# Optimization experiments

Measured on AMD Instinct MI355X. Metric: run time of the kernel, lower is better.

## Reference

```python
import jax, jax.numpy as jnp
import numpy as np

EMB_DIM = 2048
USER_DIM = 16 + 112  # 128
NUM_EXPERTS = 64
TOP_K = 8
N_TOKENS = 131072


def setup_inputs() -> dict:
    key = jax.random.key(0)
    k1, k2, k3, k4 = jax.random.split(key, 4)
    h = jax.random.normal(k1, (N_TOKENS, EMB_DIM), dtype=jnp.float32)
    u = jax.random.normal(k2, (N_TOKENS, USER_DIM), dtype=jnp.float32)
    fan_in = EMB_DIM + USER_DIM
    bound = 1.0 / np.sqrt(fan_in)
    # nn.Linear params: weight [E, emb+user], bias [E]
    W = jax.random.uniform(k3, (NUM_EXPERTS, fan_in), minval=-bound, maxval=bound, dtype=jnp.float32)
    b = jax.random.uniform(k4, (NUM_EXPERTS,), minval=-bound, maxval=bound, dtype=jnp.float32)
    return {"h": h, "u": u, "W": W, "b": b}


def reference(h, u, W, b):
    # router logits: concat along feature dim then linear -> [N, E]
    x = jnp.concatenate([h, u], axis=-1)
    g = jnp.einsum("nf,ef->ne", x, W) + b
    w = jax.nn.softmax(g, axis=-1)
    E = w.shape[-1]
    k = TOP_K
    if k is not None and k > 0 and k < E:
        _, idx = jax.lax.top_k(w, k)                      # [N, k] int32
        mask = jax.nn.one_hot(idx, E, dtype=w.dtype).sum(-2)  # [N, E] 0/1
        w = w * mask
        w = w / (w.sum(axis=-1, keepdims=True) + 1e-9)
    return w
```

## Files before the change

### kernel.cpp

```cpp
#include <hip/hip_runtime.h>
#include <math.h>

#define NTOK 131072
#define EMB  2048
#define UDIM 128
#define KDIM 2176
#define NE   64
#define TOPK 8

#define BM     128
#define BK     64
#define NCHUNK 34
#define NKSTEP 68
#define LSTR   65
#define MARGIN 1e-4f
#define WPLANE ((size_t)NKSTEP * 64 * 32)

typedef short bf16x8 __attribute__((ext_vector_type(8)));
typedef float f32x4  __attribute__((ext_vector_type(4)));

union FragU { uint4 u; bf16x8 v; };

__device__ __forceinline__ unsigned rnbf(unsigned u) {
    return u + 0x7FFFu + ((u >> 16) & 1u);
}

__device__ __forceinline__ void cvt8(const float4 a, const float4 b,
                                     uint4& hi, uint4& lo) {
    const float x[8] = {a.x, a.y, a.z, a.w, b.x, b.y, b.z, b.w};
    unsigned hh[4], ll[4];
    #pragma unroll
    for (int p = 0; p < 4; ++p) {
        const unsigned u0 = __float_as_uint(x[2*p]);
        const unsigned u1 = __float_as_uint(x[2*p+1]);
        const unsigned r0 = rnbf(u0), r1 = rnbf(u1);
        hh[p] = (r0 >> 16) | (r1 & 0xFFFF0000u);
        const float h0 = __uint_as_float(r0 & 0xFFFF0000u);
        const float h1 = __uint_as_float(r1 & 0xFFFF0000u);
        const unsigned s0 = rnbf(__float_as_uint(x[2*p]   - h0));
        const unsigned s1 = rnbf(__float_as_uint(x[2*p+1] - h1));
        ll[p] = (s0 >> 16) | (s1 & 0xFFFF0000u);
    }
    hi = make_uint4(hh[0], hh[1], hh[2], hh[3]);
    lo = make_uint4(ll[0], ll[1], ll[2], ll[3]);
}

__global__ __launch_bounds__(256)
void prep_w(const float* __restrict__ W,
            unsigned short* __restrict__ wh,
            unsigned short* __restrict__ wl)
{
    const int t = blockIdx.x * 256 + threadIdx.x;
    if (t >= NKSTEP * 64 * 4) return;
    const int lk = t & 3, e = (t >> 2) & 63, ks = t >> 8;
    const float* p = W + (size_t)e * KDIM + ks * 32 + lk * 8;
    const float4 a = *reinterpret_cast<const float4*>(p);
    const float4 c = *reinterpret_cast<const float4*>(p + 4);
    uint4 hi, lo;
    cvt8(a, c, hi, lo);
    const size_t di = ((size_t)ks * 64 + e) * 32 + lk * 8;
    *reinterpret_cast<uint4*>(wh + di) = hi;
    *reinterpret_cast<uint4*>(wl + di) = lo;
}

__global__ void zero_flags(int* flagbuf) {
    if (threadIdx.x == 0 && blockIdx.x == 0) flagbuf[0] = 0;
}

__global__ __launch_bounds__(256)
void gate_main(const float* __restrict__ h,
               const float* __restrict__ u,
               const unsigned short* __restrict__ wh,
               const unsigned short* __restrict__ wl,
               const float* __restrict__ b,
               int* __restrict__ flagbuf,
               float* __restrict__ out)
{
    __shared__ __align__(16) float ls[BM * LSTR];
    __shared__ int flaglist[BM];
    __shared__ int nflag;

    const int tid  = threadIdx.x;
    const int lane = tid & 63;
    const int wid  = tid >> 6;
    const int bm   = blockIdx.x * BM;
    const int lrow = lane & 15;
    const int lk   = lane >> 4;

    if (tid == 0) nflag = 0;

    f32x4 acc[2][4];
    #pragma unroll
    for (int mi = 0; mi < 2; ++mi)
        #pragma unroll
        for (int ni = 0; ni < 4; ++ni)
            acc[mi][ni] = (f32x4){0.f, 0.f, 0.f, 0.f};

    auto loadX = [&](int c, float4 xr[8]) {
        const bool  fh  = (c < 32);
        const float* src = fh ? h : u;
        const int   ld  = fh ? EMB : UDIM;
        const int   kb  = c * BK - (fh ? 0 : EMB);
        #pragma unroll
        for (int mi = 0; mi < 2; ++mi) {
            const size_t ro = (size_t)(bm + wid*32 + mi*16 + lrow) * ld + kb + lk*8;
            #pragma unroll
            for (int s = 0; s < 2; ++s) {
                xr[mi*4 + s*2 + 0] = *reinterpret_cast<const float4*>(src + ro + s*32);
                xr[mi*4 + s*2 + 1] = *reinterpret_cast<const float4*>(src + ro + s*32 + 4);
            }
        }
    };

    auto compute = [&](const float4 xr[8], int c) {
        #pragma unroll
        for (int s = 0; s < 2; ++s) {
            const int ks = c*2 + s;
            const uint4* bH = reinterpret_cast<const uint4*>(wh + (size_t)ks * 2048);
            const uint4* bL = reinterpret_cast<const uint4*>(wl + (size_t)ks * 2048);
            FragU bh[4], bl[4];
            #pragma unroll
            for (int ni = 0; ni < 4; ++ni) {
                const int off = (ni*16 + lrow)*4 + lk;
                bh[ni].u = bH[off];
                bl[ni].u = bL[off];
            }
            #pragma unroll
            for (int mi = 0; mi < 2; ++mi) {
                FragU ah, al;
                cvt8(xr[mi*4 + s*2], xr[mi*4 + s*2 + 1], ah.u, al.u);
                #pragma unroll
                for (int ni = 0; ni < 4; ++ni) {
                    acc[mi][ni] = __builtin_amdgcn_mfma_f32_16x16x32_bf16(ah.v, bh[ni].v, acc[mi][ni], 0, 0, 0);
                    acc[mi][ni] = __builtin_amdgcn_mfma_f32_16x16x32_bf16(ah.v, bl[ni].v, acc[mi][ni], 0, 0, 0);
                    acc[mi][ni] = __builtin_amdgcn_mfma_f32_16x16x32_bf16(al.v, bh[ni].v, acc[mi][ni], 0, 0, 0);
                }
            }
        }
    };

    float4 xcur[8], xnxt[8];
    loadX(0, xcur);
    for (int c = 0; c < NCHUNK; ++c) {
        if (c + 1 < NCHUNK) loadX(c + 1, xnxt);
        compute(xcur, c);
        #pragma unroll
        for (int i = 0; i < 8; ++i) xcur[i] = xnxt[i];
    }

    #pragma unroll
    for (int mi = 0; mi < 2; ++mi)
        #pragma unroll
        for (int ni = 0; ni < 4; ++ni) {
            const float be = b[ni*16 + lrow];
            #pragma unroll
            for (int r = 0; r < 4; ++r) {
                const int tl = wid*32 + mi*16 + lk*4 + r;
                const int e  = ni*16 + lrow;
                ls[tl * LSTR + e] = acc[mi][ni][r] + be;
            }
        }
    __syncthreads();

    if (tid < BM) {
        float* row = ls + tid * LSTR;
        unsigned long long selm = 0ULL;
        float mx = 0.f, l8 = 0.f, l9 = 0.f;
        for (int s = 0; s < TOPK + 1; ++s) {
            float best = -1e30f; int bi = 0;
            #pragma unroll
            for (int e = 0; e < NE; ++e) {
                const float v = row[e];
                if (!((selm >> e) & 1ULL) && v > best) { best = v; bi = e; }
            }
            if (s == 0) mx = best;
            if (s < TOPK) selm |= 1ULL << bi;
            if (s == TOPK - 1) l8 = best;
            if (s == TOPK)     l9 = best;
        }
        if (l8 - l9 < MARGIN) {
            const int slot = atomicAdd(&nflag, 1);
            flaglist[slot] = tid;
        }
        float tot = 0.f, s8 = 0.f;
        #pragma unroll
        for (int e = 0; e < NE; ++e) {
            const float p = __expf(row[e] - mx);
            tot += p;
            if ((selm >> e) & 1ULL) s8 += p;
            row[e] = p;
        }
        const float inv = 1.f / (s8 + 1e-9f * tot);
        #pragma unroll
        for (int e = 0; e < NE; ++e)
            row[e] = ((selm >> e) & 1ULL) ? row[e] * inv : 0.f;
    }
    __syncthreads();

    {
        const int tx = tid & 15, ty = tid >> 4;
        #pragma unroll
        for (int r = 0; r < 8; ++r) {
            const int m = ty + r * 16;
            float4 v;
            v.x = ls[m * LSTR + tx*4 + 0];
            v.y = ls[m * LSTR + tx*4 + 1];
            v.z = ls[m * LSTR + tx*4 + 2];
            v.w = ls[m * LSTR + tx*4 + 3];
            *reinterpret_cast<float4*>(out + (size_t)(bm + m) * NE + tx*4) = v;
        }
    }

    if (tid < nflag) {
        const int slot = atomicAdd(flagbuf, 1);
        flagbuf[1 + slot] = bm + flaglist[tid];
    }
}

__global__ __launch_bounds__(256)
void gate_refine(const float* __restrict__ h,
                 const float* __restrict__ u,
                 const float* __restrict__ W,
                 const float* __restrict__ b,
                 const int* __restrict__ flagbuf,
                 float* __restrict__ out)
{
    __shared__ double dscr[576];
    const int nf = flagbuf[0];
    for (int f = blockIdx.x; f < nf; f += gridDim.x) {
        const int tok  = flagbuf[1 + f];
        const int tid  = threadIdx.x;
        const int e    = tid & 63;
        const int part = tid >> 6;
        const int ka = part * 544, kb2 = ka + 544;
        double s = 0.0;
        #pragma unroll 4
        for (int k = ka; k < kb2; ++k) {
            const float xv = (k < EMB) ? h[(size_t)tok * EMB + k]
                                       : u[(size_t)tok * UDIM + (k - EMB)];
            s = fma((double)xv, (double)W[(size_t)e * KDIM + k], s);
        }
        dscr[part * 64 + e] = s;
        __syncthreads();
        if (tid < NE) {
            const double l = dscr[tid] + dscr[64 + tid] + dscr[128 + tid] +
                             dscr[192 + tid] + (double)b[tid];
            dscr[512 + tid] = l;
        }
        __syncthreads();
        if (tid == 0) {
            double* dl = dscr + 512;
            double mx = dl[0];
            #pragma unroll
            for (int e2 = 1; e2 < NE; ++e2) mx = fmax(mx, dl[e2]);
            double tot = 0.0;
            #pragma unroll
            for (int e2 = 0; e2 < NE; ++e2) {
                const double p = exp(dl[e2] - mx);
                dl[e2] = p;
                tot += p;
            }
            double s8 = 0.0;
            for (int ss = 0; ss < TOPK; ++ss) {
                double best = -1.0; int bi = 0;
                for (int e2 = 0; e2 < NE; ++e2) {
                    const double p = dl[e2];
                    if (p > best) { best = p; bi = e2; }
                }
                s8 += best;
                dl[bi] = -best;
            }
            const double inv = 1.0 / (s8 + 1e-9 * tot);
            for (int e2 = 0; e2 < NE; ++e2) {
                const double p = dl[e2];
                out[(size_t)tok * NE + e2] = (float)((p < 0.0) ? (-p) * inv : 0.0);
            }
        }
        __syncthreads();
    }
}

extern "C" void kernel_launch(void* const* d_in, const int* in_sizes, int n_in,
                              void* d_out, int out_size, void* d_ws, size_t ws_size,
                              hipStream_t stream) {
    const float* h = (const float*)d_in[0];
    const float* u = (const float*)d_in[1];
    const float* W = (const float*)d_in[2];
    const float* b = (const float*)d_in[3];
    float* out = (float*)d_out;
    (void)in_sizes; (void)n_in; (void)out_size; (void)ws_size;

    unsigned short* wh = (unsigned short*)d_ws;
    unsigned short* wl = wh + WPLANE;
    int* flagbuf = (int*)(wl + WPLANE);

    hipLaunchKernelGGL(zero_flags, dim3(1), dim3(64), 0, stream, flagbuf);
    hipLaunchKernelGGL(prep_w, dim3(NKSTEP), dim3(256), 0, stream, W, wh, wl);
    hipLaunchKernelGGL(gate_main, dim3(NTOK / BM), dim3(256), 0, stream,
                       h, u, wh, wl, b, flagbuf, out);
    hipLaunchKernelGGL(gate_refine, dim3(256), dim3(256), 0, stream,
                       h, u, W, b, flagbuf, out);
}
```

Before: 438.5 us.

## Use 512-thread blocks with one 16-row tile per wave and ping-pong X prefetch

The main gating kernel now runs 8 waves per 128-token block instead of 4. Each wave handles 16 rows rather than 32, which halves the accumulators and the prefetched X registers per thread. The single prefetch buffer is replaced by an A/B ping-pong that issues each load right after the compute that frees its registers. The aim is more waves in flight to hide global-load latency on this bandwidth-bound GEMM, at the cost of each wave now loading the W fragments for only 16 rows, so W fragment traffic doubles.

```diff
diff --git a/kernel.cpp b/kernel.cpp
--- a/kernel.cpp
+++ b/kernel.cpp
@@ -67,7 +67,7 @@
     if (threadIdx.x == 0 && blockIdx.x == 0) flagbuf[0] = 0;
 }
 
-__global__ __launch_bounds__(256)
+__global__ __launch_bounds__(512, 4)
 void gate_main(const float* __restrict__ h,
                const float* __restrict__ u,
                const unsigned short* __restrict__ wh,
@@ -89,30 +89,24 @@
 
     if (tid == 0) nflag = 0;
 
-    f32x4 acc[2][4];
+    f32x4 acc[4];
     #pragma unroll
-    for (int mi = 0; mi < 2; ++mi)
-        #pragma unroll
-        for (int ni = 0; ni < 4; ++ni)
-            acc[mi][ni] = (f32x4){0.f, 0.f, 0.f, 0.f};
-
-    auto loadX = [&](int c, float4 xr[8]) {
+    for (int ni = 0; ni < 4; ++ni)
+        acc[ni] = (f32x4){0.f, 0.f, 0.f, 0.f};
+
+    auto loadX = [&](int c, float4 xr[4]) {
         const bool  fh  = (c < 32);
         const float* src = fh ? h : u;
         const int   ld  = fh ? EMB : UDIM;
         const int   kb  = c * BK - (fh ? 0 : EMB);
-        #pragma unroll
-        for (int mi = 0; mi < 2; ++mi) {
-            const size_t ro = (size_t)(bm + wid*32 + mi*16 + lrow) * ld + kb + lk*8;
-            #pragma unroll
-            for (int s = 0; s < 2; ++s) {
-                xr[mi*4 + s*2 + 0] = *reinterpret_cast<const float4*>(src + ro + s*32);
-                xr[mi*4 + s*2 + 1] = *reinterpret_cast<const float4*>(src + ro + s*32 + 4);
-            }
-        }
+        const size_t ro = (size_t)(bm + wid*16 + lrow) * ld + kb + lk*8;
+        xr[0] = *reinterpret_cast<const float4*>(src + ro);
+        xr[1] = *reinterpret_cast<const float4*>(src + ro + 4);
+        xr[2] = *reinterpret_cast<const float4*>(src + ro + 32);
+        xr[3] = *reinterpret_cast<const float4*>(src + ro + 36);
     };
 
-    auto compute = [&](const float4 xr[8], int c) {
+    auto compute = [&](const float4 xr[4], int c) {
         #pragma unroll
         for (int s = 0; s < 2; ++s) {
             const int ks = c*2 + s;
@@ -125,41 +119,38 @@
                 bh[ni].u = bH[off];
                 bl[ni].u = bL[off];
             }
-            #pragma unroll
-            for (int mi = 0; mi < 2; ++mi) {
-                FragU ah, al;
-                cvt8(xr[mi*4 + s*2], xr[mi*4 + s*2 + 1], ah.u, al.u);
-                #pragma unroll
-                for (int ni = 0; ni < 4; ++ni) {
-                    acc[mi][ni] = __builtin_amdgcn_mfma_f32_16x16x32_bf16(ah.v, bh[ni].v, acc[mi][ni], 0, 0, 0);
-                    acc[mi][ni] = __builtin_amdgcn_mfma_f32_16x16x32_bf16(ah.v, bl[ni].v, acc[mi][ni], 0, 0, 0);
-                    acc[mi][ni] = __builtin_amdgcn_mfma_f32_16x16x32_bf16(al.v, bh[ni].v, acc[mi][ni], 0, 0, 0);
-                }
+            FragU ah, al;
+            cvt8(xr[s*2], xr[s*2 + 1], ah.u, al.u);
+            #pragma unroll
+            for (int ni = 0; ni < 4; ++ni) {
+                acc[ni] = __builtin_amdgcn_mfma_f32_16x16x32_bf16(ah.v, bh[ni].v, acc[ni], 0, 0, 0);
+                acc[ni] = __builtin_amdgcn_mfma_f32_16x16x32_bf16(ah.v, bl[ni].v, acc[ni], 0, 0, 0);
+                acc[ni] = __builtin_amdgcn_mfma_f32_16x16x32_bf16(al.v, bh[ni].v, acc[ni], 0, 0, 0);
             }
         }
     };
 
-    float4 xcur[8], xnxt[8];
-    loadX(0, xcur);
-    for (int c = 0; c < NCHUNK; ++c) {
-        if (c + 1 < NCHUNK) loadX(c + 1, xnxt);
-        compute(xcur, c);
-        #pragma unroll
-        for (int i = 0; i < 8; ++i) xcur[i] = xnxt[i];
-    }
+    float4 xA[4], xB[4];
+    loadX(0, xA);
+    loadX(1, xB);
+    for (int c = 0; c < 32; c += 2) {
+        compute(xA, c);
+        loadX(c + 2, xA);
+        compute(xB, c + 1);
+        loadX(c + 3, xB);
+    }
+    compute(xA, 32);
+    compute(xB, 33);
 
     #pragma unroll
-    for (int mi = 0; mi < 2; ++mi)
-        #pragma unroll
-        for (int ni = 0; ni < 4; ++ni) {
-            const float be = b[ni*16 + lrow];
-            #pragma unroll
-            for (int r = 0; r < 4; ++r) {
-                const int tl = wid*32 + mi*16 + lk*4 + r;
-                const int e  = ni*16 + lrow;
-                ls[tl * LSTR + e] = acc[mi][ni][r] + be;
-            }
-        }
+    for (int ni = 0; ni < 4; ++ni) {
+        const float be = b[ni*16 + lrow];
+        #pragma unroll
+        for (int r = 0; r < 4; ++r) {
+            const int tl = wid*16 + lk*4 + r;
+            ls[tl * LSTR + ni*16 + lrow] = acc[ni][r] + be;
+        }
+    }
     __syncthreads();
 
     if (tid < BM) {
@@ -200,8 +191,8 @@
     {
         const int tx = tid & 15, ty = tid >> 4;
         #pragma unroll
-        for (int r = 0; r < 8; ++r) {
-            const int m = ty + r * 16;
+        for (int r = 0; r < 4; ++r) {
+            const int m = ty + r * 32;
             float4 v;
             v.x = ls[m * LSTR + tx*4 + 0];
             v.y = ls[m * LSTR + tx*4 + 1];
@@ -296,7 +287,7 @@
 
     hipLaunchKernelGGL(zero_flags, dim3(1), dim3(64), 0, stream, flagbuf);
     hipLaunchKernelGGL(prep_w, dim3(NKSTEP), dim3(256), 0, stream, W, wh, wl);
-    hipLaunchKernelGGL(gate_main, dim3(NTOK / BM), dim3(256), 0, stream,
+    hipLaunchKernelGGL(gate_main, dim3(NTOK / BM), dim3(512), 0, stream,
                        h, u, wh, wl, b, flagbuf, out);
     hipLaunchKernelGGL(gate_refine, dim3(256), dim3(256), 0, stream,
                        h, u, W, b, flagbuf, out);
```

New measurement: 543.0 us. 23.8% more time.

## Deepen X prefetch to four k-steps and double-buffer weight fragments

Applied to the files above, without the earlier changes.

Restructures the GEMM main loop so X rows are prefetched four k-steps ahead in a rotating register ring, and the bf16 weight fragments are double-buffered one step ahead. Each step loads the next weights, converts the current X, and issues the next X load before the MFMAs. The goal is to hide global memory latency for the streamed h/u activations, which dominate this memory-bound kernel. The cost is more live registers, which may lower occupancy.

```diff
diff --git a/kernel.cpp b/kernel.cpp
--- a/kernel.cpp
+++ b/kernel.cpp
@@ -9,8 +9,6 @@
 #define TOPK 8
 
 #define BM     128
-#define BK     64
-#define NCHUNK 34
 #define NKSTEP 68
 #define LSTR   65
 #define MARGIN 1e-4f
@@ -96,57 +94,73 @@
         for (int ni = 0; ni < 4; ++ni)
             acc[mi][ni] = (f32x4){0.f, 0.f, 0.f, 0.f};
 
-    auto loadX = [&](int c, float4 xr[8]) {
-        const bool  fh  = (c < 32);
-        const float* src = fh ? h : u;
-        const int   ld  = fh ? EMB : UDIM;
-        const int   kb  = c * BK - (fh ? 0 : EMB);
+    FragU  wf[2][8];
+    float4 x[4][4];
+
+    auto wfLoad = [&](int ks, FragU* wfb) {
+        const uint4* bH = reinterpret_cast<const uint4*>(wh + (size_t)ks * 2048);
+        const uint4* bL = reinterpret_cast<const uint4*>(wl + (size_t)ks * 2048);
+        #pragma unroll
+        for (int ni = 0; ni < 4; ++ni) {
+            const int off = (ni*16 + lrow)*4 + lk;
+            wfb[ni]    .u = bH[off];
+            wfb[4 + ni].u = bL[off];
+        }
+    };
+    auto xLoad = [&](int ks, float4* xb, int src) {
+        const float* s  = src ? u : h;
+        const int    ld = src ? UDIM : EMB;
+        const int    col = ks*32 - (src ? EMB : 0) + lk*8;
         #pragma unroll
         for (int mi = 0; mi < 2; ++mi) {
-            const size_t ro = (size_t)(bm + wid*32 + mi*16 + lrow) * ld + kb + lk*8;
-            #pragma unroll
-            for (int s = 0; s < 2; ++s) {
-                xr[mi*4 + s*2 + 0] = *reinterpret_cast<const float4*>(src + ro + s*32);
-                xr[mi*4 + s*2 + 1] = *reinterpret_cast<const float4*>(src + ro + s*32 + 4);
-            }
+            const size_t ro = (size_t)(bm + wid*32 + mi*16 + lrow) * ld + col;
+            xb[mi*2 + 0] = *reinterpret_cast<const float4*>(s + ro);
+            xb[mi*2 + 1] = *reinterpret_cast<const float4*>(s + ro + 4);
         }
     };
 
-    auto compute = [&](const float4 xr[8], int c) {
-        #pragma unroll
-        for (int s = 0; s < 2; ++s) {
-            const int ks = c*2 + s;
-            const uint4* bH = reinterpret_cast<const uint4*>(wh + (size_t)ks * 2048);
-            const uint4* bL = reinterpret_cast<const uint4*>(wl + (size_t)ks * 2048);
-            FragU bh[4], bl[4];
-            #pragma unroll
-            for (int ni = 0; ni < 4; ++ni) {
-                const int off = (ni*16 + lrow)*4 + lk;
-                bh[ni].u = bH[off];
-                bl[ni].u = bL[off];
-            }
-            #pragma unroll
-            for (int mi = 0; mi < 2; ++mi) {
-                FragU ah, al;
-                cvt8(xr[mi*4 + s*2], xr[mi*4 + s*2 + 1], ah.u, al.u);
-                #pragma unroll
-                for (int ni = 0; ni < 4; ++ni) {
-                    acc[mi][ni] = __builtin_amdgcn_mfma_f32_16x16x32_bf16(ah.v, bh[ni].v, acc[mi][ni], 0, 0, 0);
-                    acc[mi][ni] = __builtin_amdgcn_mfma_f32_16x16x32_bf16(ah.v, bl[ni].v, acc[mi][ni], 0, 0, 0);
-                    acc[mi][ni] = __builtin_amdgcn_mfma_f32_16x16x32_bf16(al.v, bh[ni].v, acc[mi][ni], 0, 0, 0);
-                }
-            }
-        }
-    };
-
-    float4 xcur[8], xnxt[8];
-    loadX(0, xcur);
-    for (int c = 0; c < NCHUNK; ++c) {
-        if (c + 1 < NCHUNK) loadX(c + 1, xnxt);
-        compute(xcur, c);
-        #pragma unroll
-        for (int i = 0; i < 8; ++i) xcur[i] = xnxt[i];
-    }
+#define PHASE(I, KS, WNEXT, XSRC) do {                                          \
+    if (WNEXT) wfLoad((KS) + 1, wf[((I) + 1) & 1]);                             \
+    FragU ah0, al0, ah1, al1;                                                   \
+    cvt8(x[(I) & 3][0], x[(I) & 3][1], ah0.u, al0.u);                           \
+    cvt8(x[(I) & 3][2], x[(I) & 3][3], ah1.u, al1.u);                           \
+    if ((XSRC) >= 0) xLoad((KS) + 4, x[(I) & 3], (XSRC));                       \
+    FragU* wc = wf[(I) & 1];                                                    \
+    _Pragma("unroll")                                                           \
+    for (int ni = 0; ni < 4; ++ni) {                                            \
+        acc[0][ni] = __builtin_amdgcn_mfma_f32_16x16x32_bf16(ah0.v, wc[ni].v,     acc[0][ni], 0, 0, 0); \
+        acc[0][ni] = __builtin_amdgcn_mfma_f32_16x16x32_bf16(ah0.v, wc[4+ni].v,   acc[0][ni], 0, 0, 0); \
+        acc[0][ni] = __builtin_amdgcn_mfma_f32_16x16x32_bf16(al0.v, wc[ni].v,     acc[0][ni], 0, 0, 0); \
+        acc[1][ni] = __builtin_amdgcn_mfma_f32_16x16x32_bf16(ah1.v, wc[ni].v,     acc[1][ni], 0, 0, 0); \
+        acc[1][ni] = __builtin_amdgcn_mfma_f32_16x16x32_bf16(ah1.v, wc[4+ni].v,   acc[1][ni], 0, 0, 0); \
+        acc[1][ni] = __builtin_amdgcn_mfma_f32_16x16x32_bf16(al1.v, wc[ni].v,     acc[1][ni], 0, 0, 0); \
+    }                                                                           \
+} while (0)
+
+    wfLoad(0, wf[0]);
+    xLoad(0, x[0], 0);
+    xLoad(1, x[1], 0);
+    xLoad(2, x[2], 0);
+    xLoad(3, x[3], 0);
+
+    #pragma unroll 1
+    for (int g = 0; g < 15; ++g) {
+        const int ks = g * 4;
+        PHASE(0, ks + 0, 1, 0);
+        PHASE(1, ks + 1, 1, 0);
+        PHASE(2, ks + 2, 1, 0);
+        PHASE(3, ks + 3, 1, 0);
+    }
+    PHASE(0, 60, 1, 1);
+    PHASE(1, 61, 1, 1);
+    PHASE(2, 62, 1, 1);
+    PHASE(3, 63, 1, 1);
+    PHASE(0, 64, 1, -1);
+    PHASE(1, 65, 1, -1);
+    PHASE(2, 66, 1, -1);
+    PHASE(3, 67, 0, -1);
+
+#undef PHASE
 
     #pragma unroll
     for (int mi = 0; mi < 2; ++mi)
```

After: 528.2 us. 1.2x slower.

## Stage gate weights into LDS via direct global-to-LDS loads with double buffering

Applied to the files above, without the earlier changes.

Weight hi/lo bf16 planes are now copied into a double-buffered shared-memory region using global_load_lds, replacing per-wave global loads of B fragments, and prep_w writes them in a lane-contiguous fragment order so each lane reads one uint4. The X register prefetch is restructured to a single register set, loaded mid-chunk after conversion, and launch bounds now request 4 blocks per CU. This is meant to cut redundant L2 traffic for the weights and lower register pressure. In exchange it adds a block-wide barrier every chunk and less lookahead for the X loads.

```diff
diff --git a/kernel.cpp b/kernel.cpp
--- a/kernel.cpp
+++ b/kernel.cpp
@@ -45,6 +45,12 @@
     lo = make_uint4(ll[0], ll[1], ll[2], ll[3]);
 }
 
+__device__ __forceinline__ void gll16(const void* gsrc, void* ldst) {
+    __builtin_amdgcn_global_load_lds(
+        (const __attribute__((address_space(1))) void*)gsrc,
+        (__attribute__((address_space(3))) void*)ldst, 16, 0, 0);
+}
+
 __global__ __launch_bounds__(256)
 void prep_w(const float* __restrict__ W,
             unsigned short* __restrict__ wh,
@@ -58,7 +64,8 @@
     const float4 c = *reinterpret_cast<const float4*>(p + 4);
     uint4 hi, lo;
     cvt8(a, c, hi, lo);
-    const size_t di = ((size_t)ks * 64 + e) * 32 + lk * 8;
+    const size_t di = (size_t)ks * 2048 +
+                      ((size_t)((e >> 4) * 64 + (e & 15) + 16 * lk)) * 8;
     *reinterpret_cast<uint4*>(wh + di) = hi;
     *reinterpret_cast<uint4*>(wl + di) = lo;
 }
@@ -67,7 +74,7 @@
     if (threadIdx.x == 0 && blockIdx.x == 0) flagbuf[0] = 0;
 }
 
-__global__ __launch_bounds__(256)
+__global__ __launch_bounds__(256, 4)
 void gate_main(const float* __restrict__ h,
                const float* __restrict__ u,
                const unsigned short* __restrict__ wh,
@@ -76,7 +83,7 @@
                int* __restrict__ flagbuf,
                float* __restrict__ out)
 {
-    __shared__ __align__(16) float ls[BM * LSTR];
+    __shared__ __align__(16) char smem[33536];
     __shared__ int flaglist[BM];
     __shared__ int nflag;
 
@@ -96,7 +103,9 @@
         for (int ni = 0; ni < 4; ++ni)
             acc[mi][ni] = (f32x4){0.f, 0.f, 0.f, 0.f};
 
-    auto loadX = [&](int c, float4 xr[8]) {
+    float4 xr[8];
+
+    auto loadX = [&](int c) {
         const bool  fh  = (c < 32);
         const float* src = fh ? h : u;
         const int   ld  = fh ? EMB : UDIM;
@@ -112,42 +121,55 @@
         }
     };
 
-    auto compute = [&](const float4 xr[8], int c) {
+    auto stageW = [&](int c, int pb) {
+        const char* hsrc = (const char*)wh + (size_t)c * 8192;
+        const char* lsrc = (const char*)wl + (size_t)c * 8192;
+        char* dst = smem + pb * 16384;
+        #pragma unroll
+        for (int i = 0; i < 2; ++i) {
+            const int o = wid * 2048 + i * 1024;
+            gll16(hsrc + o + lane * 16, dst + o);
+            gll16(lsrc + o + lane * 16, dst + 8192 + o);
+        }
+    };
+
+    auto computeChunk = [&](int c, int pb) {
+        const uint4* wb = reinterpret_cast<const uint4*>(smem + pb * 16384);
         #pragma unroll
         for (int s = 0; s < 2; ++s) {
-            const int ks = c*2 + s;
-            const uint4* bH = reinterpret_cast<const uint4*>(wh + (size_t)ks * 2048);
-            const uint4* bL = reinterpret_cast<const uint4*>(wl + (size_t)ks * 2048);
             FragU bh[4], bl[4];
             #pragma unroll
             for (int ni = 0; ni < 4; ++ni) {
-                const int off = (ni*16 + lrow)*4 + lk;
-                bh[ni].u = bH[off];
-                bl[ni].u = bL[off];
-            }
-            #pragma unroll
-            for (int mi = 0; mi < 2; ++mi) {
-                FragU ah, al;
-                cvt8(xr[mi*4 + s*2], xr[mi*4 + s*2 + 1], ah.u, al.u);
+                bh[ni].u = wb[s*256 + ni*64 + lane];
+                bl[ni].u = wb[512 + s*256 + ni*64 + lane];
+            }
+            FragU ah[2], al[2];
+            cvt8(xr[0*4 + s*2], xr[0*4 + s*2 + 1], ah[0].u, al[0].u);
+            cvt8(xr[1*4 + s*2], xr[1*4 + s*2 + 1], ah[1].u, al[1].u);
+            if (s == 1 && c + 1 < NCHUNK) loadX(c + 1);
+            #pragma unroll
+            for (int mi = 0; mi < 2; ++mi)
                 #pragma unroll
                 for (int ni = 0; ni < 4; ++ni) {
-                    acc[mi][ni] = __builtin_amdgcn_mfma_f32_16x16x32_bf16(ah.v, bh[ni].v, acc[mi][ni], 0, 0, 0);
-                    acc[mi][ni] = __builtin_amdgcn_mfma_f32_16x16x32_bf16(ah.v, bl[ni].v, acc[mi][ni], 0, 0, 0);
-                    acc[mi][ni] = __builtin_amdgcn_mfma_f32_16x16x32_bf16(al.v, bh[ni].v, acc[mi][ni], 0, 0, 0);
+                    acc[mi][ni] = __builtin_amdgcn_mfma_f32_16x16x32_bf16(ah[mi].v, bh[ni].v, acc[mi][ni], 0, 0, 0);
+                    acc[mi][ni] = __builtin_amdgcn_mfma_f32_16x16x32_bf16(ah[mi].v, bl[ni].v, acc[mi][ni], 0, 0, 0);
+                    acc[mi][ni] = __builtin_amdgcn_mfma_f32_16x16x32_bf16(al[mi].v, bh[ni].v, acc[mi][ni], 0, 0, 0);
                 }
-            }
         }
     };
 
-    float4 xcur[8], xnxt[8];
-    loadX(0, xcur);
+    stageW(0, 0);
+    loadX(0);
+    __syncthreads();
+
+    #pragma unroll 1
     for (int c = 0; c < NCHUNK; ++c) {
-        if (c + 1 < NCHUNK) loadX(c + 1, xnxt);
-        compute(xcur, c);
-        #pragma unroll
-        for (int i = 0; i < 8; ++i) xcur[i] = xnxt[i];
-    }
-
+        if (c + 1 < NCHUNK) stageW(c + 1, (c + 1) & 1);
+        computeChunk(c, c & 1);
+        __syncthreads();
+    }
+
+    float* ls = reinterpret_cast<float*>(smem);
     #pragma unroll
     for (int mi = 0; mi < 2; ++mi)
         #pragma unroll
```

Result: faster. 393.7 us (-10.2%).
